# Performance work log

Measured on AMD Instinct MI355X. Metric: run time of the kernel, lower is better.

The kernel has to match this reference:

```python
import jax, jax.numpy as jnp
import numpy as np

L, H, E, D, FF, V, CTX = 8, 16, 1024, 64, 4096, 2048, 2048
B, T = 4, 1024


def _ln(x, g, b, eps=1e-5):
    mu = x.mean(-1, keepdims=True)
    var = ((x - mu) ** 2).mean(-1, keepdims=True)
    return (x - mu) * jax.lax.rsqrt(var + eps) * g + b


def setup_inputs() -> dict:
    key = jax.random.key(0)
    ks = jax.random.split(key, 12)
    s = 0.02
    return {
        "tokens": jax.random.randint(ks[0], (B, T), 0, V),
        "tok_emb": jax.random.normal(ks[1], (V, E), jnp.float32) * s,
        "pos_emb": jax.random.normal(ks[2], (CTX, E), jnp.float32) * s,
        "Wq": jax.random.normal(ks[3], (L, H, E, D), jnp.float32) * s,
        "Wk": jax.random.normal(ks[4], (L, H, E, D), jnp.float32) * s,
        "Wv": jax.random.normal(ks[5], (L, H, E, D), jnp.float32) * s,
        "Wo": jax.random.normal(ks[6], (L, H * D, E), jnp.float32) * s,
        "bo": jnp.zeros((L, E), jnp.float32),
        "ln1_g": jnp.ones((L, E), jnp.float32),
        "ln1_b": jnp.zeros((L, E), jnp.float32),
        "ln2_g": jnp.ones((L, E), jnp.float32),
        "ln2_b": jnp.zeros((L, E), jnp.float32),
        "W1": jax.random.normal(ks[7], (L, E, FF), jnp.float32) * s,
        "b1": jnp.zeros((L, FF), jnp.float32),
        "W2": jax.random.normal(ks[8], (L, FF, E), jnp.float32) * s,
        "b2": jnp.zeros((L, E), jnp.float32),
        "lnf_g": jnp.ones((E,), jnp.float32),
        "lnf_b": jnp.zeros((E,), jnp.float32),
        "Wlm": jax.random.normal(ks[9], (E, V), jnp.float32) * s,
        "blm": jnp.zeros((V,), jnp.float32),
    }


def reference(tokens, tok_emb, pos_emb, Wq, Wk, Wv, Wo, bo, ln1_g, ln1_b,
              ln2_g, ln2_b, W1, b1, W2, b2, lnf_g, lnf_b, Wlm, blm):
    # NOTE: original indexes pos_embd with token ids (pos_embd(x.int()))
    x = tok_emb[tokens] + pos_emb[tokens]  # [B,T,E]
    t = x.shape[1]
    causal = jnp.tril(jnp.ones((t, t), bool))
    scale = 1.0 / jnp.sqrt(jnp.float32(D))
    for l in range(L):
        x = _ln(x, ln1_g[l], ln1_b[l])
        q = jnp.einsum('bte,hed->bhtd', x, Wq[l])
        k = jnp.einsum('bte,hed->bhtd', x, Wk[l])
        v = jnp.einsum('bte,hed->bhtd', x, Wv[l])
        scores = jnp.einsum('bhtd,bhsd->bhts', q, k) * scale
        scores = jnp.where(causal, scores, -jnp.inf)
        att = jax.nn.softmax(scores, axis=-1)
        o = jnp.einsum('bhts,bhsd->bhtd', att, v)
        o = o.transpose(0, 2, 1, 3).reshape(x.shape[0], t, H * D)
        x = x + o @ Wo[l] + bo[l]
        x = _ln(x, ln2_g[l], ln2_b[l])
        x = x + jax.nn.relu(x @ W1[l] + b1[l]) @ W2[l] + b2[l]
    x = _ln(x, lnf_g, lnf_b)
    return x @ Wlm + blm
```

## Files before the change

### kernel.cpp

```cpp
#include <hip/hip_runtime.h>
#include <hip/hip_bf16.h>

#define LAYERS 8
#define H_ 16
#define E_ 1024
#define D_ 64
#define FF_ 4096
#define V_ 2048
#define B_ 4
#define T_ 1024
#define MTOK (B_*T_)

typedef __bf16 bf16x8_t __attribute__((ext_vector_type(8)));
typedef __bf16 bf16x4_t __attribute__((ext_vector_type(4)));
typedef float f32x4_t __attribute__((ext_vector_type(4)));
typedef __hip_bfloat16 bf16_t;

__device__ __forceinline__ bf16_t f2b(float f) { return __float2bfloat16(f); }

__global__ void embed_kernel(const int* __restrict__ tokens,
                             const float* __restrict__ te,
                             const float* __restrict__ pe,
                             bf16_t* __restrict__ x) {
  int row = blockIdx.x;
  int tok = tokens[row];
  int t = threadIdx.x;
  float4 va = ((const float4*)(te + (size_t)tok * E_))[t];
  float4 vp = ((const float4*)(pe + (size_t)tok * E_))[t];
  bf16x4_t o;
  o[0] = (__bf16)(va.x + vp.x); o[1] = (__bf16)(va.y + vp.y);
  o[2] = (__bf16)(va.z + vp.z); o[3] = (__bf16)(va.w + vp.w);
  ((bf16x4_t*)(x + (size_t)row * E_))[t] = o;
}

__global__ __launch_bounds__(256) void ln_kernel(const bf16_t* __restrict__ xin,
                                                 bf16_t* __restrict__ xout,
                                                 const float* __restrict__ g,
                                                 const float* __restrict__ b) {
  int row = blockIdx.x, tid = threadIdx.x;
  bf16x4_t v4 = ((const bf16x4_t*)(xin + (size_t)row * E_))[tid];
  float v0 = (float)v4[0], v1 = (float)v4[1], v2 = (float)v4[2], v3 = (float)v4[3];
  float s  = v0 + v1 + v2 + v3;
  float sq = v0*v0 + v1*v1 + v2*v2 + v3*v3;
  for (int off = 32; off; off >>= 1) {
    s  += __shfl_xor(s, off, 64);
    sq += __shfl_xor(sq, off, 64);
  }
  __shared__ float2 wred[4];
  if ((tid & 63) == 0) wred[tid >> 6] = make_float2(s, sq);
  __syncthreads();
  float2 w0 = wred[0], w1 = wred[1], w2 = wred[2], w3 = wred[3];
  float S = w0.x + w1.x + w2.x + w3.x, SQ = w0.y + w1.y + w2.y + w3.y;
  float mean = S * (1.0f / E_);
  float var  = SQ * (1.0f / E_) - mean * mean;
  float inv = rsqrtf(var + 1e-5f);
  float4 gv = ((const float4*)g)[tid];
  float4 bv = ((const float4*)b)[tid];
  bf16x4_t o;
  o[0] = (__bf16)((v0 - mean) * inv * gv.x + bv.x);
  o[1] = (__bf16)((v1 - mean) * inv * gv.y + bv.y);
  o[2] = (__bf16)((v2 - mean) * inv * gv.z + bv.z);
  o[3] = (__bf16)((v3 - mean) * inv * gv.w + bv.w);
  ((bf16x4_t*)(xout + (size_t)row * E_))[tid] = o;
}

__global__ void transpose_kernel(const float* __restrict__ in, bf16_t* __restrict__ out,
                                 int R, int C) {
  __shared__ float tile[32][33];
  int z = blockIdx.z;
  const float* ib = in + (size_t)z * R * C;
  bf16_t* ob = out + (size_t)z * R * C;
  int r0 = blockIdx.y * 32, c0 = blockIdx.x * 32;
  int tx = threadIdx.x, ty = threadIdx.y;
  for (int i = 0; i < 4; i++)
    tile[ty + i * 8][tx] = ib[(size_t)(r0 + ty + i * 8) * C + (c0 + tx)];
  __syncthreads();
  for (int i = 0; i < 4; i++)
    ob[(size_t)(c0 + ty + i * 8) * R + (r0 + tx)] = f2b(tile[tx][ty + i * 8]);
}

enum { MODE_F32 = 0, MODE_BF16 = 1, MODE_QKV = 2 };

__device__ __forceinline__ void gload16(const bf16_t* g, bf16_t* l) {
  __builtin_amdgcn_global_load_lds((const __attribute__((address_space(1))) void*)g,
                                   (__attribute__((address_space(3))) void*)l, 16, 0, 0);
}

__device__ __forceinline__ int xcd_swz(int flat, int nwg) {
  int q = nwg >> 3, r = nwg & 7;
  int xcd = flat & 7, idx = flat >> 3;
  return (xcd < r ? xcd * (q + 1) : r * (q + 1) + (xcd - r) * q) + idx;
}

template <int BN, int MODE>
__global__ __launch_bounds__(512) void gemm256_kernel(
    const bf16_t* __restrict__ A, int lda,
    const bf16_t* __restrict__ Bt, int ldb,
    void* __restrict__ C, long long sCz,
    const float* __restrict__ bias,
    int M, int N, int kspan, int relu) {
  constexpr int NF = BN / 64;
  constexpr int MF = 8;
  constexpr int ACH = 4;
  constexpr int BCH = BN / 64;
  constexpr int LPS = ACH + BCH;
  __shared__ __align__(16) bf16_t As0[256 * 64];
  __shared__ __align__(16) bf16_t As1[256 * 64];
  __shared__ __align__(16) bf16_t Bs0[BN * 64];
  __shared__ __align__(16) bf16_t Bs1[BN * 64];
  int tid = threadIdx.x, lane = tid & 63, wave = tid >> 6;
  int wm = wave >> 2, wn = wave & 3;
  int z = blockIdx.z;
  int nwg = gridDim.x * gridDim.y;
  int flat = xcd_swz(blockIdx.y * gridDim.x + blockIdx.x, nwg);
  int m0 = (flat / gridDim.x) * 256, n0 = (flat % gridDim.x) * BN;
  const bf16_t* Ab = A + (size_t)m0 * lda + (size_t)z * kspan;
  const bf16_t* Bb = Bt + (size_t)n0 * ldb + (size_t)z * kspan;
  int sr = lane & 15, sc = (lane >> 4) * 8;

  f32x4_t acc[MF][NF];
#pragma unroll
  for (int i = 0; i < MF; i++)
#pragma unroll
    for (int j = 0; j < NF; j++)
      acc[i][j] = (f32x4_t){0.f, 0.f, 0.f, 0.f};

  auto stage = [&](bf16_t* Ad, bf16_t* Bd, int kt) {
    int kg = kt * 64;
#pragma unroll
    for (int ch = 0; ch < ACH; ch++) {
      int sub = wave * ACH + ch;
      gload16(Ab + (size_t)((sub >> 1) * 16 + sr) * lda + kg + (sub & 1) * 32 + sc,
              Ad + sub * 512);
    }
#pragma unroll
    for (int ch = 0; ch < BCH; ch++) {
      int sub = wave * BCH + ch;
      gload16(Bb + (size_t)((sub >> 1) * 16 + sr) * ldb + kg + (sub & 1) * 32 + sc,
              Bd + sub * 512);
    }
  };

  auto compute = [&](const bf16_t* Asb, const bf16_t* Bsb) {
#pragma unroll
    for (int ks = 0; ks < 2; ks++) {
      bf16x8_t af[MF], bfv[NF];
#pragma unroll
      for (int i = 0; i < MF; i++)
        af[i] = *(const bf16x8_t*)(Asb + ((wm * MF + i) * 2 + ks) * 512 + lane * 8);
#pragma unroll
      for (int j = 0; j < NF; j++)
        bfv[j] = *(const bf16x8_t*)(Bsb + ((wn * NF + j) * 2 + ks) * 512 + lane * 8);
      __builtin_amdgcn_s_setprio(1);
#pragma unroll
      for (int i = 0; i < MF; i++)
#pragma unroll
        for (int j = 0; j < NF; j++)
          acc[i][j] = __builtin_amdgcn_mfma_f32_16x16x32_bf16(af[i], bfv[j], acc[i][j], 0, 0, 0);
      __builtin_amdgcn_s_setprio(0);
    }
  };

  int nk = kspan / 64;
  stage(As0, Bs0, 0);
  stage(As1, Bs1, 1);
  for (int kt = 0; kt < nk; kt += 2) {
    asm volatile("s_waitcnt vmcnt(%0)" :: "n"(LPS) : "memory");
    __builtin_amdgcn_s_barrier();
    compute(As0, Bs0);
    __builtin_amdgcn_sched_barrier(0);
    __builtin_amdgcn_s_barrier();
    bool more = (kt + 2 < nk);
    if (more) {
      stage(As0, Bs0, kt + 2);
      asm volatile("s_waitcnt vmcnt(%0)" :: "n"(LPS) : "memory");
    } else {
      asm volatile("s_waitcnt vmcnt(0)" ::: "memory");
    }
    __builtin_amdgcn_s_barrier();
    compute(As1, Bs1);
    __builtin_amdgcn_sched_barrier(0);
    __builtin_amdgcn_s_barrier();
    if (more) stage(As1, Bs1, kt + 3);
  }

#pragma unroll
  for (int i = 0; i < MF; i++)
#pragma unroll
    for (int j = 0; j < NF; j++) {
      f32x4_t v = acc[i][j];
      int n = n0 + (wn * NF + j) * 16 + (lane & 15);
      int mb = m0 + (wm * MF + i) * 16 + (lane >> 4) * 4;
#pragma unroll
      for (int r = 0; r < 4; r++) {
        int m = mb + r;
        float val = v[r];
        if (bias) val += bias[n];
        if (relu) val = fmaxf(val, 0.f);
        if (MODE == MODE_F32) {
          size_t idx = (size_t)z * sCz + (size_t)m * N + n;
          ((float*)C)[idx] = val;
        } else if (MODE == MODE_BF16) {
          size_t idx = (size_t)z * sCz + (size_t)m * N + n;
          ((bf16_t*)C)[idx] = f2b(val);
        } else {
          int sect = n >> 10, hd = n & 1023, h = hd >> 6, d = hd & 63;
          int b = m >> 10, t = m & 1023;
          size_t base = (size_t)sect * ((size_t)B_ * H_ * T_ * D_);
          size_t idx = base + ((size_t)(b * H_ + h) << 16) +
                       (sect == 2 ? (size_t)((d << 10) + t) : (size_t)((t << 6) + d));
          ((bf16_t*)C)[idx] = f2b(val);
        }
      }
    }
}

template <int NS>
__global__ __launch_bounds__(256) void splitk_reduce_kernel(const bf16_t* __restrict__ p,
                                                            const bf16_t* __restrict__ t,
                                                            bf16_t* __restrict__ r,
                                                            const float* __restrict__ bias) {
  size_t i = (size_t)blockIdx.x * 256 + threadIdx.x;
  bf16x8_t tv = ((const bf16x8_t*)t)[i];
  int base = (int)((i * 8) & (E_ - 1));
  float acc[8];
#pragma unroll
  for (int j = 0; j < 8; j++) acc[j] = (float)tv[j] + bias[base + j];
#pragma unroll
  for (int s = 0; s < NS; s++) {
    bf16x8_t pv = ((const bf16x8_t*)p)[i + (size_t)s * ((size_t)MTOK * E_ / 8)];
#pragma unroll
    for (int j = 0; j < 8; j++) acc[j] += (float)pv[j];
  }
  bf16x8_t ov;
#pragma unroll
  for (int j = 0; j < 8; j++) ov[j] = (__bf16)acc[j];
  ((bf16x8_t*)r)[i] = ov;
}

#define KPAD 72

__global__ __launch_bounds__(256) void flash_kernel(
    const bf16_t* __restrict__ q,
    const bf16_t* __restrict__ kk,
    const bf16_t* __restrict__ vt,
    bf16_t* __restrict__ o) {
  __shared__ __align__(16) bf16_t Ks[64 * KPAD];
  __shared__ __align__(16) bf16_t Vs[64 * KPAD];
  __shared__ __align__(16) bf16_t Ps[4][16 * KPAD];
  int bid = blockIdx.x;
  int qi = 15 - (bid >> 6);
  int bh = bid & 63;
  int b = bh >> 4, h = bh & 15;
  const bf16_t* qb = q + ((size_t)bh << 16);
  const bf16_t* kb = kk + ((size_t)bh << 16);
  const bf16_t* vb = vt + ((size_t)bh << 16);
  int tid = threadIdx.x, lane = tid & 63, wave = tid >> 6;
  int lr = lane & 15, lg = lane >> 4;
  int qbase = qi * 64;

  bf16x8_t qf[2];
  {
    const bf16_t* qrow = qb + (size_t)(qbase + wave * 16 + lr) * D_ + lg * 8;
    qf[0] = *(const bf16x8_t*)(qrow);
    qf[1] = *(const bf16x8_t*)(qrow + 32);
  }

  float m_r[4], l_r[4];
  f32x4_t oc[4];
#pragma unroll
  for (int r = 0; r < 4; r++) { m_r[r] = -1e30f; l_r[r] = 0.f; }
#pragma unroll
  for (int j = 0; j < 4; j++) oc[j] = (f32x4_t){0.f, 0.f, 0.f, 0.f};

  int srow = tid >> 2, scol = (tid & 3) * 16;

  bf16x8_t k0, k1, v0, v1;
  {
    const bf16_t* kg = kb + (size_t)srow * D_ + scol;
    k0 = *(const bf16x8_t*)kg;
    k1 = *(const bf16x8_t*)(kg + 8);
    const bf16_t* vg = vb + (size_t)srow * T_ + scol;
    v0 = *(const bf16x8_t*)vg;
    v1 = *(const bf16x8_t*)(vg + 8);
  }

  for (int s = 0; s <= qi; s++) {
    __syncthreads();
    *(bf16x8_t*)(&Ks[srow * KPAD + scol]) = k0;
    *(bf16x8_t*)(&Ks[srow * KPAD + scol + 8]) = k1;
    *(bf16x8_t*)(&Vs[srow * KPAD + scol]) = v0;
    *(bf16x8_t*)(&Vs[srow * KPAD + scol + 8]) = v1;
    __syncthreads();

    if (s < qi) {
      int kv1 = (s + 1) * 64;
      const bf16_t* kg = kb + (size_t)(kv1 + srow) * D_ + scol;
      k0 = *(const bf16x8_t*)kg;
      k1 = *(const bf16x8_t*)(kg + 8);
      const bf16_t* vg = vb + (size_t)srow * T_ + kv1 + scol;
      v0 = *(const bf16x8_t*)vg;
      v1 = *(const bf16x8_t*)(vg + 8);
    }

    int kv0 = s * 64;
    f32x4_t sc[4];
#pragma unroll
    for (int j = 0; j < 4; j++) {
      f32x4_t a = (f32x4_t){0.f, 0.f, 0.f, 0.f};
      bf16x8_t b0 = *(const bf16x8_t*)(&Ks[(j * 16 + lr) * KPAD + lg * 8]);
      bf16x8_t b1 = *(const bf16x8_t*)(&Ks[(j * 16 + lr) * KPAD + lg * 8 + 32]);
      a = __builtin_amdgcn_mfma_f32_16x16x32_bf16(qf[0], b0, a, 0, 0, 0);
      a = __builtin_amdgcn_mfma_f32_16x16x32_bf16(qf[1], b1, a, 0, 0, 0);
      sc[j] = a;
    }
    if (s == qi) {
#pragma unroll
      for (int j = 0; j < 4; j++)
#pragma unroll
        for (int r = 0; r < 4; r++) {
          int kvp = kv0 + j * 16 + lr;
          int qp  = qbase + wave * 16 + lg * 4 + r;
          sc[j][r] = (kvp <= qp) ? sc[j][r] * 0.125f : -1e30f;
        }
    } else {
#pragma unroll
      for (int j = 0; j < 4; j++)
#pragma unroll
        for (int r = 0; r < 4; r++) sc[j][r] *= 0.125f;
    }

    float ex[4];
#pragma unroll
    for (int r = 0; r < 4; r++) {
      float v = fmaxf(fmaxf(sc[0][r], sc[1][r]), fmaxf(sc[2][r], sc[3][r]));
      v = fmaxf(v, __shfl_xor(v, 1, 64));
      v = fmaxf(v, __shfl_xor(v, 2, 64));
      v = fmaxf(v, __shfl_xor(v, 4, 64));
      v = fmaxf(v, __shfl_xor(v, 8, 64));
      float mn = fmaxf(m_r[r], v);
      ex[r] = __expf(m_r[r] - mn);
      m_r[r] = mn;
      l_r[r] *= ex[r];
    }
#pragma unroll
    for (int j = 0; j < 4; j++)
#pragma unroll
      for (int r = 0; r < 4; r++) {
        float p = __expf(sc[j][r] - m_r[r]);
        l_r[r] += p;
        Ps[wave][(lg * 4 + r) * KPAD + j * 16 + lr] = f2b(p);
      }

#pragma unroll
    for (int j = 0; j < 4; j++)
#pragma unroll
      for (int r = 0; r < 4; r++) oc[j][r] *= ex[r];

    bf16x8_t pa0 = *(const bf16x8_t*)(&Ps[wave][lr * KPAD + lg * 8]);
    bf16x8_t pa1 = *(const bf16x8_t*)(&Ps[wave][lr * KPAD + lg * 8 + 32]);
#pragma unroll
    for (int j = 0; j < 4; j++) {
      bf16x8_t vb0 = *(const bf16x8_t*)(&Vs[(j * 16 + lr) * KPAD + lg * 8]);
      bf16x8_t vb1 = *(const bf16x8_t*)(&Vs[(j * 16 + lr) * KPAD + lg * 8 + 32]);
      oc[j] = __builtin_amdgcn_mfma_f32_16x16x32_bf16(pa0, vb0, oc[j], 0, 0, 0);
      oc[j] = __builtin_amdgcn_mfma_f32_16x16x32_bf16(pa1, vb1, oc[j], 0, 0, 0);
    }
  }

#pragma unroll
  for (int r = 0; r < 4; r++) {
    float v = l_r[r];
    v += __shfl_xor(v, 1, 64);
    v += __shfl_xor(v, 2, 64);
    v += __shfl_xor(v, 4, 64);
    v += __shfl_xor(v, 8, 64);
    l_r[r] = 1.f / v;
  }
  bf16_t* ob = o + ((size_t)(b * T_ + qbase + wave * 16)) * (H_ * D_) + h * D_;
#pragma unroll
  for (int j = 0; j < 4; j++)
#pragma unroll
    for (int r = 0; r < 4; r++) {
      int qrow = lg * 4 + r;
      ob[(size_t)qrow * (H_ * D_) + j * 16 + lr] = f2b(oc[j][r] * l_r[r]);
    }
}

extern "C" void kernel_launch(void* const* d_in, const int* in_sizes, int n_in,
                              void* d_out, int out_size, void* d_ws, size_t ws_size,
                              hipStream_t stream) {
  (void)in_sizes; (void)n_in; (void)out_size; (void)ws_size;
  const int*   tokens = (const int*)d_in[0];
  const float* tok_emb = (const float*)d_in[1];
  const float* pos_emb = (const float*)d_in[2];
  const float* Wq = (const float*)d_in[3];
  const float* Wk = (const float*)d_in[4];
  const float* Wv = (const float*)d_in[5];
  const float* Wo = (const float*)d_in[6];
  const float* bo = (const float*)d_in[7];
  const float* ln1_g = (const float*)d_in[8];
  const float* ln1_b = (const float*)d_in[9];
  const float* ln2_g = (const float*)d_in[10];
  const float* ln2_b = (const float*)d_in[11];
  const float* W1 = (const float*)d_in[12];
  const float* b1 = (const float*)d_in[13];
  const float* W2 = (const float*)d_in[14];
  const float* b2 = (const float*)d_in[15];
  const float* lnf_g = (const float*)d_in[16];
  const float* lnf_b = (const float*)d_in[17];
  const float* Wlm = (const float*)d_in[18];
  const float* blm = (const float*)d_in[19];

  char* w = (char*)d_ws;
  size_t off = 0;
  auto alloc = [&](size_t bytes) { void* p = (void*)(w + off); off += (bytes + 255) & ~(size_t)255; return p; };
  bf16_t* r    = (bf16_t*)alloc((size_t)MTOK * E_ * 2);
  bf16_t* t    = (bf16_t*)alloc((size_t)MTOK * E_ * 2);
  bf16_t* q    = (bf16_t*)alloc((size_t)B_ * H_ * T_ * D_ * 2);
  bf16_t* kk   = (bf16_t*)alloc((size_t)B_ * H_ * T_ * D_ * 2);
  bf16_t* vt   = (bf16_t*)alloc((size_t)B_ * H_ * T_ * D_ * 2);
  bf16_t* o    = (bf16_t*)alloc((size_t)MTOK * E_ * 2);
  bf16_t* h1   = (bf16_t*)alloc((size_t)MTOK * FF_ * 2);
  bf16_t* WqkvT = (bf16_t*)alloc((size_t)3 * E_ * H_ * D_ * 2);
  bf16_t* WoT  = (bf16_t*)alloc((size_t)E_ * H_ * D_ * 2);
  bf16_t* W1T  = (bf16_t*)alloc((size_t)E_ * FF_ * 2);
  bf16_t* W2T  = (bf16_t*)alloc((size_t)E_ * FF_ * 2);
  bf16_t* WlmT = (bf16_t*)alloc((size_t)E_ * V_ * 2);
  bf16_t* p2   = (bf16_t*)alloc((size_t)2 * MTOK * E_ * 2);

  embed_kernel<<<MTOK, 256, 0, stream>>>(tokens, tok_emb, pos_emb, r);
  transpose_kernel<<<dim3(V_ / 32, E_ / 32, 1), dim3(32, 8), 0, stream>>>(Wlm, WlmT, E_, V_);

  for (int l = 0; l < LAYERS; l++) {
    ln_kernel<<<MTOK, 256, 0, stream>>>(r, t, ln1_g + l * E_, ln1_b + l * E_);

    transpose_kernel<<<dim3(D_ / 32, E_ / 32, H_), dim3(32, 8), 0, stream>>>(
        Wq + (size_t)l * H_ * E_ * D_, WqkvT, E_, D_);
    transpose_kernel<<<dim3(D_ / 32, E_ / 32, H_), dim3(32, 8), 0, stream>>>(
        Wk + (size_t)l * H_ * E_ * D_, WqkvT + (size_t)E_ * H_ * D_, E_, D_);
    transpose_kernel<<<dim3(D_ / 32, E_ / 32, H_), dim3(32, 8), 0, stream>>>(
        Wv + (size_t)l * H_ * E_ * D_, WqkvT + (size_t)2 * E_ * H_ * D_, E_, D_);
    transpose_kernel<<<dim3(E_ / 32, (H_ * D_) / 32, 1), dim3(32, 8), 0, stream>>>(
        Wo + (size_t)l * H_ * D_ * E_, WoT, H_ * D_, E_);
    transpose_kernel<<<dim3(FF_ / 32, E_ / 32, 1), dim3(32, 8), 0, stream>>>(
        W1 + (size_t)l * E_ * FF_, W1T, E_, FF_);
    transpose_kernel<<<dim3(E_ / 32, FF_ / 32, 1), dim3(32, 8), 0, stream>>>(
        W2 + (size_t)l * FF_ * E_, W2T, FF_, E_);

    gemm256_kernel<256, MODE_QKV><<<dim3(12, 16, 1), 512, 0, stream>>>(
        t, E_, WqkvT, E_, q, 0, nullptr, MTOK, 3 * H_ * D_, E_, 0);

    flash_kernel<<<1024, 256, 0, stream>>>(q, kk, vt, o);

    gemm256_kernel<128, MODE_BF16><<<dim3(8, 16, 2), 512, 0, stream>>>(
        o, H_ * D_, WoT, H_ * D_, p2, (long long)MTOK * E_, nullptr,
        MTOK, E_, (H_ * D_) / 2, 0);
    splitk_reduce_kernel<2><<<MTOK * E_ / 2048, 256, 0, stream>>>(p2, t, r, bo + l * E_);

    ln_kernel<<<MTOK, 256, 0, stream>>>(r, t, ln2_g + l * E_, ln2_b + l * E_);

    gemm256_kernel<256, MODE_BF16><<<dim3(16, 16, 1), 512, 0, stream>>>(
        t, E_, W1T, E_, h1, 0, b1 + l * FF_, MTOK, FF_, E_, 1);
    gemm256_kernel<128, MODE_BF16><<<dim3(8, 16, 2), 512, 0, stream>>>(
        h1, FF_, W2T, FF_, p2, (long long)MTOK * E_, nullptr, MTOK, E_, FF_ / 2, 0);
    splitk_reduce_kernel<2><<<MTOK * E_ / 2048, 256, 0, stream>>>(p2, t, r, b2 + l * E_);
  }

  ln_kernel<<<MTOK, 256, 0, stream>>>(r, t, lnf_g, lnf_b);
  gemm256_kernel<128, MODE_F32><<<dim3(16, 16, 1), 512, 0, stream>>>(
      t, E_, WlmT, E_, d_out, 0, blm, MTOK, V_, E_, 0);
}
```

Measured before the change: 2.411 ms.

## Rewrite GEMM with triple-buffered LDS pipeline and fixed 256x128 tiles

Replaces the double-buffered 256xBN GEMM with a single 256x128-tile kernel that uses three LDS buffers. Global-to-LDS loads for tile t+2 are issued in halves inside each compute phase, and fragments are read with explicit ds_read_b128 so memory traffic overlaps MFMA work with fewer barriers per k-step. The QKV and W1 GEMMs now launch twice as many workgroups with smaller N tiles. This trades more A-tile reloads and a larger LDS footprint (144KB) for deeper prefetch and more workgroups.

```diff
diff --git a/kernel.cpp b/kernel.cpp
--- a/kernel.cpp
+++ b/kernel.cpp
@@ -92,105 +92,95 @@
   return (xcd < r ? xcd * (q + 1) : r * (q + 1) + (xcd - r) * q) + idx;
 }
 
-template <int BN, int MODE>
-__global__ __launch_bounds__(512) void gemm256_kernel(
+template <int MODE>
+__global__ __launch_bounds__(512) void gemm3_kernel(
     const bf16_t* __restrict__ A, int lda,
     const bf16_t* __restrict__ Bt, int ldb,
     void* __restrict__ C, long long sCz,
     const float* __restrict__ bias,
     int M, int N, int kspan, int relu) {
-  constexpr int NF = BN / 64;
-  constexpr int MF = 8;
-  constexpr int ACH = 4;
-  constexpr int BCH = BN / 64;
-  constexpr int LPS = ACH + BCH;
-  __shared__ __align__(16) bf16_t As0[256 * 64];
-  __shared__ __align__(16) bf16_t As1[256 * 64];
-  __shared__ __align__(16) bf16_t Bs0[BN * 64];
-  __shared__ __align__(16) bf16_t Bs1[BN * 64];
+  constexpr int ABUFE = 256 * 64;
+  constexpr int BBUFE = 128 * 64;
+  __shared__ __align__(16) bf16_t LA[3 * ABUFE];
+  __shared__ __align__(16) bf16_t LB[3 * BBUFE];
   int tid = threadIdx.x, lane = tid & 63, wave = tid >> 6;
-  int wm = wave >> 2, wn = wave & 3;
+  int wm = wave >> 1, wn = wave & 1;
   int z = blockIdx.z;
   int nwg = gridDim.x * gridDim.y;
   int flat = xcd_swz(blockIdx.y * gridDim.x + blockIdx.x, nwg);
-  int m0 = (flat / gridDim.x) * 256, n0 = (flat % gridDim.x) * BN;
+  int m0 = (flat / gridDim.x) * 256, n0 = (flat % gridDim.x) * 128;
   const bf16_t* Ab = A + (size_t)m0 * lda + (size_t)z * kspan;
   const bf16_t* Bb = Bt + (size_t)n0 * ldb + (size_t)z * kspan;
   int sr = lane & 15, sc = (lane >> 4) * 8;
 
-  f32x4_t acc[MF][NF];
-#pragma unroll
-  for (int i = 0; i < MF; i++)
-#pragma unroll
-    for (int j = 0; j < NF; j++)
+  f32x4_t acc[4][4];
+#pragma unroll
+  for (int i = 0; i < 4; i++)
+#pragma unroll
+    for (int j = 0; j < 4; j++)
       acc[i][j] = (f32x4_t){0.f, 0.f, 0.f, 0.f};
 
-  auto stage = [&](bf16_t* Ad, bf16_t* Bd, int kt) {
+  auto stageh = [&](int b, int kt, int h) {
     int kg = kt * 64;
 #pragma unroll
-    for (int ch = 0; ch < ACH; ch++) {
-      int sub = wave * ACH + ch;
+    for (int ch = 0; ch < 2; ch++) {
+      int sub = wave * 4 + 2 * h + ch;
       gload16(Ab + (size_t)((sub >> 1) * 16 + sr) * lda + kg + (sub & 1) * 32 + sc,
-              Ad + sub * 512);
-    }
-#pragma unroll
-    for (int ch = 0; ch < BCH; ch++) {
-      int sub = wave * BCH + ch;
+              LA + b * ABUFE + sub * 512);
+    }
+    {
+      int sub = wave * 2 + h;
       gload16(Bb + (size_t)((sub >> 1) * 16 + sr) * ldb + kg + (sub & 1) * 32 + sc,
-              Bd + sub * 512);
+              LB + b * BBUFE + sub * 512);
     }
   };
 
-  auto compute = [&](const bf16_t* Asb, const bf16_t* Bsb) {
-#pragma unroll
-    for (int ks = 0; ks < 2; ks++) {
-      bf16x8_t af[MF], bfv[NF];
-#pragma unroll
-      for (int i = 0; i < MF; i++)
-        af[i] = *(const bf16x8_t*)(Asb + ((wm * MF + i) * 2 + ks) * 512 + lane * 8);
-#pragma unroll
-      for (int j = 0; j < NF; j++)
-        bfv[j] = *(const bf16x8_t*)(Bsb + ((wn * NF + j) * 2 + ks) * 512 + lane * 8);
-      __builtin_amdgcn_s_setprio(1);
-#pragma unroll
-      for (int i = 0; i < MF; i++)
-#pragma unroll
-        for (int j = 0; j < NF; j++)
-          acc[i][j] = __builtin_amdgcn_mfma_f32_16x16x32_bf16(af[i], bfv[j], acc[i][j], 0, 0, 0);
-      __builtin_amdgcn_s_setprio(0);
-    }
+  auto phase = [&](int b, int ks, int t, int nk) {
+    bf16x8_t af[4], bfv[4];
+    unsigned abase = (unsigned)(size_t)(LA + b * ABUFE);
+    unsigned bbase = (unsigned)(size_t)(LB + b * BBUFE);
+#pragma unroll
+    for (int i = 0; i < 4; i++) {
+      unsigned ad = abase + (unsigned)((((wm * 4 + i) * 2 + ks) * 512 + lane * 8) * 2);
+      asm volatile("ds_read_b128 %0, %1" : "=v"(af[i]) : "v"(ad));
+    }
+#pragma unroll
+    for (int j = 0; j < 4; j++) {
+      unsigned bd = bbase + (unsigned)((((wn * 4 + j) * 2 + ks) * 512 + lane * 8) * 2);
+      asm volatile("ds_read_b128 %0, %1" : "=v"(bfv[j]) : "v"(bd));
+    }
+    if (t + 2 < nk) stageh((t + 2) % 3, t + 2, ks);
+    __builtin_amdgcn_s_barrier();
+    asm volatile("s_waitcnt lgkmcnt(0)" ::: "memory");
+    __builtin_amdgcn_sched_barrier(0);
+    __builtin_amdgcn_s_setprio(1);
+#pragma unroll
+    for (int i = 0; i < 4; i++)
+#pragma unroll
+      for (int j = 0; j < 4; j++)
+        acc[i][j] = __builtin_amdgcn_mfma_f32_16x16x32_bf16(af[i], bfv[j], acc[i][j], 0, 0, 0);
+    __builtin_amdgcn_s_setprio(0);
   };
 
   int nk = kspan / 64;
-  stage(As0, Bs0, 0);
-  stage(As1, Bs1, 1);
-  for (int kt = 0; kt < nk; kt += 2) {
-    asm volatile("s_waitcnt vmcnt(%0)" :: "n"(LPS) : "memory");
+  stageh(0, 0, 0); stageh(0, 0, 1);
+  stageh(1, 1, 0); stageh(1, 1, 1);
+  for (int t = 0; t < nk; ++t) {
+    int b = t % 3;
+    if (t + 1 < nk) { asm volatile("s_waitcnt vmcnt(6)" ::: "memory"); }
+    else            { asm volatile("s_waitcnt vmcnt(0)" ::: "memory"); }
     __builtin_amdgcn_s_barrier();
-    compute(As0, Bs0);
-    __builtin_amdgcn_sched_barrier(0);
-    __builtin_amdgcn_s_barrier();
-    bool more = (kt + 2 < nk);
-    if (more) {
-      stage(As0, Bs0, kt + 2);
-      asm volatile("s_waitcnt vmcnt(%0)" :: "n"(LPS) : "memory");
-    } else {
-      asm volatile("s_waitcnt vmcnt(0)" ::: "memory");
-    }
-    __builtin_amdgcn_s_barrier();
-    compute(As1, Bs1);
-    __builtin_amdgcn_sched_barrier(0);
-    __builtin_amdgcn_s_barrier();
-    if (more) stage(As1, Bs1, kt + 3);
-  }
-
-#pragma unroll
-  for (int i = 0; i < MF; i++)
-#pragma unroll
-    for (int j = 0; j < NF; j++) {
+    phase(b, 0, t, nk);
+    phase(b, 1, t, nk);
+  }
+
+#pragma unroll
+  for (int i = 0; i < 4; i++)
+#pragma unroll
+    for (int j = 0; j < 4; j++) {
       f32x4_t v = acc[i][j];
-      int n = n0 + (wn * NF + j) * 16 + (lane & 15);
-      int mb = m0 + (wm * MF + i) * 16 + (lane >> 4) * 4;
+      int n = n0 + wn * 64 + j * 16 + (lane & 15);
+      int mb = m0 + wm * 64 + i * 16 + (lane >> 4) * 4;
 #pragma unroll
       for (int r = 0; r < 4; r++) {
         int m = mb + r;
@@ -205,10 +195,10 @@
           ((bf16_t*)C)[idx] = f2b(val);
         } else {
           int sect = n >> 10, hd = n & 1023, h = hd >> 6, d = hd & 63;
-          int b = m >> 10, t = m & 1023;
+          int b2 = m >> 10, tt = m & 1023;
           size_t base = (size_t)sect * ((size_t)B_ * H_ * T_ * D_);
-          size_t idx = base + ((size_t)(b * H_ + h) << 16) +
-                       (sect == 2 ? (size_t)((d << 10) + t) : (size_t)((t << 6) + d));
+          size_t idx = base + ((size_t)(b2 * H_ + h) << 16) +
+                       (sect == 2 ? (size_t)((d << 10) + tt) : (size_t)((tt << 6) + d));
           ((bf16_t*)C)[idx] = f2b(val);
         }
       }
@@ -448,26 +438,26 @@
     transpose_kernel<<<dim3(E_ / 32, FF_ / 32, 1), dim3(32, 8), 0, stream>>>(
         W2 + (size_t)l * FF_ * E_, W2T, FF_, E_);
 
-    gemm256_kernel<256, MODE_QKV><<<dim3(12, 16, 1), 512, 0, stream>>>(
+    gemm3_kernel<MODE_QKV><<<dim3(24, 16, 1), 512, 0, stream>>>(
         t, E_, WqkvT, E_, q, 0, nullptr, MTOK, 3 * H_ * D_, E_, 0);
 
     flash_kernel<<<1024, 256, 0, stream>>>(q, kk, vt, o);
 
-    gemm256_kernel<128, MODE_BF16><<<dim3(8, 16, 2), 512, 0, stream>>>(
+    gemm3_kernel<MODE_BF16><<<dim3(8, 16, 2), 512, 0, stream>>>(
         o, H_ * D_, WoT, H_ * D_, p2, (long long)MTOK * E_, nullptr,
         MTOK, E_, (H_ * D_) / 2, 0);
     splitk_reduce_kernel<2><<<MTOK * E_ / 2048, 256, 0, stream>>>(p2, t, r, bo + l * E_);
 
     ln_kernel<<<MTOK, 256, 0, stream>>>(r, t, ln2_g + l * E_, ln2_b + l * E_);
 
-    gemm256_kernel<256, MODE_BF16><<<dim3(16, 16, 1), 512, 0, stream>>>(
+    gemm3_kernel<MODE_BF16><<<dim3(32, 16, 1), 512, 0, stream>>>(
         t, E_, W1T, E_, h1, 0, b1 + l * FF_, MTOK, FF_, E_, 1);
-    gemm256_kernel<128, MODE_BF16><<<dim3(8, 16, 2), 512, 0, stream>>>(
+    gemm3_kernel<MODE_BF16><<<dim3(8, 16, 2), 512, 0, stream>>>(
         h1, FF_, W2T, FF_, p2, (long long)MTOK * E_, nullptr, MTOK, E_, FF_ / 2, 0);
     splitk_reduce_kernel<2><<<MTOK * E_ / 2048, 256, 0, stream>>>(p2, t, r, b2 + l * E_);
   }
 
   ln_kernel<<<MTOK, 256, 0, stream>>>(r, t, lnf_g, lnf_b);
-  gemm256_kernel<128, MODE_F32><<<dim3(16, 16, 1), 512, 0, stream>>>(
+  gemm3_kernel<MODE_F32><<<dim3(16, 16, 1), 512, 0, stream>>>(
       t, E_, WlmT, E_, d_out, 0, blm, MTOK, V_, E_, 0);
 }
```

After: 2.277 ms. 1.06x faster.
